# Performance work log

Measured on AMD Instinct MI355X. Metric: run time of the kernel, lower is better.

## Reference

```python
import jax, jax.numpy as jnp
import numpy as np

EPS = 1e-8  # torch.nn.CosineSimilarity default eps


def setup_inputs() -> dict:
    key = jax.random.key(0)
    k1, k2, k3 = jax.random.split(key, 3)
    B, D, C = 262144, 256, 64
    inputs = jax.random.normal(k1, (B, D), dtype=jnp.float32)
    labels = jax.random.randint(k2, (B,), 0, C, dtype=jnp.int64)
    class_avgs = jax.random.normal(k3, (C, D), dtype=jnp.float32)
    return {"inputs": inputs, "labels": labels, "class_avgs": class_avgs}


def reference(inputs, labels, class_avgs):
    # Cosine similarity of every input row against every class centroid.
    # Faithful to the original double loop: classes whose avg vector contains
    # inf get similarity 1.0 (the "unseen class" sentinel branch).
    inf_mask = jnp.any(jnp.isinf(class_avgs), axis=-1)  # (C,)
    x_norm = jnp.linalg.norm(inputs, axis=-1)           # (B,)
    c_norm = jnp.linalg.norm(class_avgs, axis=-1)       # (C,)
    dots = jnp.einsum("bd,cd->bc", inputs, class_avgs)  # (B, C)
    denom = jnp.maximum(x_norm[:, None] * c_norm[None, :], EPS)
    sims = dots / denom
    return jnp.where(inf_mask[None, :], jnp.float32(1.0), sims)
```

## Files before the change

kernel.cpp:

```cpp
#include <hip/hip_runtime.h>
#include <hip/hip_bf16.h>


typedef __attribute__((ext_vector_type(8))) short bf16x8;
typedef __attribute__((ext_vector_type(4))) float f32x4;

#define EPS 1e-8f

__device__ __forceinline__ short f2bf(float f) {
  union { float f; unsigned u; } v; v.f = f;
  unsigned r = v.u + 0x7fffu + ((v.u >> 16) & 1u);
  return (short)(r >> 16);
}

__global__ __launch_bounds__(256) void simrel_kernel(
    const float* __restrict__ X,
    const float* __restrict__ CLS,
    float* __restrict__ OUT)
{
  constexpr int D  = 256;
  constexpr int C  = 64;
  constexpr int SK = 264;

  __shared__ __align__(16) short Blds[C * SK];
  __shared__ float cn_s[C];
  __shared__ float cinf_s[C];

  const int tid = threadIdx.x;

  {
    const int c = tid >> 2;
    const int q = tid & 3;
    const float4* src = (const float4*)(CLS + c * D + q * 64);
    short* dst = &Blds[c * SK + q * 64];
    float ssq = 0.f;
    int inf = 0;
#pragma unroll
    for (int i = 0; i < 16; ++i) {
      float4 v = src[i];
      ssq += v.x * v.x + v.y * v.y;
      ssq += v.z * v.z + v.w * v.w;
      inf |= (isinf(v.x) | isinf(v.y) | isinf(v.z) | isinf(v.w));
      *(short4*)(dst + i * 4) =
          make_short4(f2bf(v.x), f2bf(v.y), f2bf(v.z), f2bf(v.w));
    }
    ssq += __shfl_xor(ssq, 1);
    ssq += __shfl_xor(ssq, 2);
    inf |= __shfl_xor(inf, 1);
    inf |= __shfl_xor(inf, 2);
    if (q == 0) {
      cn_s[c]   = sqrtf(ssq);
      cinf_s[c] = inf ? 1.f : 0.f;
    }
  }
  __syncthreads();

  const int lane = tid & 63;
  const int wave = tid >> 6;
  const int m    = lane & 15;
  const int quad = lane >> 4;

  const long rowbase = (long)blockIdx.x * 256 + wave * 64;

  const float4* Ap[4];
#pragma unroll
  for (int mt = 0; mt < 4; ++mt)
    Ap[mt] = (const float4*)X + (rowbase + mt * 16 + m) * 64 + quad * 2;

  const short* Bp[4];
#pragma unroll
  for (int nt = 0; nt < 4; ++nt)
    Bp[nt] = &Blds[(nt * 16 + m) * SK + quad * 8];

  f32x4 acc[4][4];
#pragma unroll
  for (int mt = 0; mt < 4; ++mt)
#pragma unroll
    for (int nt = 0; nt < 4; ++nt)
      acc[mt][nt] = (f32x4){0.f, 0.f, 0.f, 0.f};

  float ssqr[4] = {0.f, 0.f, 0.f, 0.f};

  float4 cur[8];
#pragma unroll
  for (int mt = 0; mt < 4; ++mt) {
    cur[2 * mt]     = Ap[mt][0];
    cur[2 * mt + 1] = Ap[mt][1];
  }

#pragma unroll
  for (int ks = 0; ks < 8; ++ks) {
    float4 nxt[8];
    if (ks < 7) {
#pragma unroll
      for (int mt = 0; mt < 4; ++mt) {
        nxt[2 * mt]     = Ap[mt][(ks + 1) * 8];
        nxt[2 * mt + 1] = Ap[mt][(ks + 1) * 8 + 1];
      }
    }

    bf16x8 bf[4];
#pragma unroll
    for (int nt = 0; nt < 4; ++nt)
      bf[nt] = *(const bf16x8*)(Bp[nt] + ks * 32);

#pragma unroll
    for (int mt = 0; mt < 4; ++mt) {
      float4 a0 = cur[2 * mt], a1 = cur[2 * mt + 1];
      ssqr[mt] += a0.x * a0.x + a0.y * a0.y + a0.z * a0.z + a0.w * a0.w +
                  a1.x * a1.x + a1.y * a1.y + a1.z * a1.z + a1.w * a1.w;
      bf16x8 af;
      af[0] = f2bf(a0.x); af[1] = f2bf(a0.y); af[2] = f2bf(a0.z); af[3] = f2bf(a0.w);
      af[4] = f2bf(a1.x); af[5] = f2bf(a1.y); af[6] = f2bf(a1.z); af[7] = f2bf(a1.w);
#pragma unroll
      for (int nt = 0; nt < 4; ++nt)
        acc[mt][nt] =
            __builtin_amdgcn_mfma_f32_16x16x32_bf16(af, bf[nt], acc[mt][nt], 0, 0, 0);
    }

    if (ks < 7) {
#pragma unroll
      for (int i = 0; i < 8; ++i) cur[i] = nxt[i];
    }
  }

#pragma unroll
  for (int mt = 0; mt < 4; ++mt) {
    float s = ssqr[mt];
    s += __shfl_xor(s, 16);
    s += __shfl_xor(s, 32);
    float xn = sqrtf(s);
    float xnr[4];
#pragma unroll
    for (int r = 0; r < 4; ++r)
      xnr[r] = __shfl(xn, quad * 4 + r);
#pragma unroll
    for (int nt = 0; nt < 4; ++nt) {
      const int n = nt * 16 + m;
      const float cn  = cn_s[n];
      const bool cinf = (cinf_s[n] != 0.f);
#pragma unroll
      for (int r = 0; r < 4; ++r) {
        const long row = rowbase + mt * 16 + quad * 4 + r;
        const float denom = fmaxf(xnr[r] * cn, EPS);
        const float v =
            cinf ? 1.0f : acc[mt][nt][r] * __builtin_amdgcn_rcpf(denom);
        OUT[row * 64 + n] = v;
      }
    }
  }
}

extern "C" void kernel_launch(void* const* d_in, const int* in_sizes, int n_in,
                              void* d_out, int out_size, void* d_ws, size_t ws_size,
                              hipStream_t stream) {
  (void)n_in; (void)d_ws; (void)ws_size; (void)out_size;
  const float* X   = (const float*)d_in[0];
  const float* CLS = (const float*)d_in[2];
  float* OUT = (float*)d_out;

  const int Brows  = in_sizes[0] / 256;
  const int blocks = Brows / 256;
  simrel_kernel<<<blocks, 256, 0, stream>>>(X, CLS, OUT);
}
```

Baseline: 392.9 us.

## Stream input rows via global_load_lds double buffer and pre-swizzle class fragments

Input tiles are now fetched straight into per-wave LDS double buffers with global_load_lds and explicit vmcnt waits, instead of register prefetch. Class centroids are stored in LDS in MFMA fragment order, and their norms and inf flags are recomputed per wave from the bf16 copies. Each block now handles 128 rows instead of 256, which lowers register pressure but repeats the centroid setup more often. Computing the centroid norm from bf16 values slightly changes accuracy.

```diff
diff --git a/kernel.cpp b/kernel.cpp
--- a/kernel.cpp
+++ b/kernel.cpp
@@ -1,5 +1,6 @@
 #include <hip/hip_runtime.h>
 #include <hip/hip_bf16.h>
+#include <math.h>
 
 
 typedef __attribute__((ext_vector_type(8))) short bf16x8;
@@ -12,121 +13,133 @@
   unsigned r = v.u + 0x7fffu + ((v.u >> 16) & 1u);
   return (short)(r >> 16);
 }
+__device__ __forceinline__ float bf2f(short s) {
+  union { float f; unsigned u; } v;
+  v.u = ((unsigned)(unsigned short)s) << 16;
+  return v.f;
+}
+
+__device__ __forceinline__ void dma16(const float* g, float* l) {
+  __builtin_amdgcn_global_load_lds(
+      (const __attribute__((address_space(1))) void*)g,
+      (__attribute__((address_space(3))) void*)l, 16, 0, 0);
+}
+
 
 __global__ __launch_bounds__(256) void simrel_kernel(
     const float* __restrict__ X,
     const float* __restrict__ CLS,
     float* __restrict__ OUT)
 {
-  constexpr int D  = 256;
-  constexpr int C  = 64;
-  constexpr int SK = 264;
+  __shared__ __align__(16) float Abuf[4 * 2048];
+  __shared__ __align__(16) short Bfrag[8 * 4 * 64 * 8];
 
-  __shared__ __align__(16) short Blds[C * SK];
-  __shared__ float cn_s[C];
-  __shared__ float cinf_s[C];
-
-  const int tid = threadIdx.x;
+  const int tid  = threadIdx.x;
+  const int wave = tid >> 6;
+  const int lane = tid & 63;
+  const int m    = lane & 15;
+  const int quad = lane >> 4;
 
   {
-    const int c = tid >> 2;
-    const int q = tid & 3;
-    const float4* src = (const float4*)(CLS + c * D + q * 64);
-    short* dst = &Blds[c * SK + q * 64];
-    float ssq = 0.f;
-    int inf = 0;
+    const int c  = tid >> 2;
+    const int qq = tid & 3;
+    const float4* src = (const float4*)CLS + c * 64 + qq * 16;
 #pragma unroll
     for (int i = 0; i < 16; ++i) {
       float4 v = src[i];
-      ssq += v.x * v.x + v.y * v.y;
-      ssq += v.z * v.z + v.w * v.w;
-      inf |= (isinf(v.x) | isinf(v.y) | isinf(v.z) | isinf(v.w));
-      *(short4*)(dst + i * 4) =
+      const int wabs = qq * 64 + i * 4;
+      const int ks = wabs >> 5;
+      const int w0 = wabs & 31;
+      const int h  = w0 >> 4;
+      const int qd = (w0 >> 2) & 3;
+      const int lb = (qd << 4) | (c & 15);
+      const int nt = c >> 4;
+      *(short4*)&Bfrag[((ks * 4 + nt) * 64 + lb) * 8 + h * 4] =
           make_short4(f2bf(v.x), f2bf(v.y), f2bf(v.z), f2bf(v.w));
-    }
-    ssq += __shfl_xor(ssq, 1);
-    ssq += __shfl_xor(ssq, 2);
-    inf |= __shfl_xor(inf, 1);
-    inf |= __shfl_xor(inf, 2);
-    if (q == 0) {
-      cn_s[c]   = sqrtf(ssq);
-      cinf_s[c] = inf ? 1.f : 0.f;
     }
   }
   __syncthreads();
 
-  const int lane = tid & 63;
-  const int wave = tid >> 6;
-  const int m    = lane & 15;
-  const int quad = lane >> 4;
+  const size_t rowbase = (size_t)blockIdx.x * 128 + (size_t)wave * 32;
 
-  const long rowbase = (long)blockIdx.x * 256 + wave * 64;
+  const float* gbase[2][2];
+#pragma unroll
+  for (int mti = 0; mti < 2; ++mti)
+#pragma unroll
+    for (int h = 0; h < 2; ++h)
+      gbase[mti][h] = X + (rowbase + mti * 16 + m) * 256 + h * 16 + quad * 4;
 
-  const float4* Ap[4];
+  float* abase = &Abuf[wave * 2048];
+
 #pragma unroll
-  for (int mt = 0; mt < 4; ++mt)
-    Ap[mt] = (const float4*)X + (rowbase + mt * 16 + m) * 64 + quad * 2;
+  for (int mti = 0; mti < 2; ++mti)
+#pragma unroll
+    for (int h = 0; h < 2; ++h)
+      dma16(gbase[mti][h], abase + (mti * 2 + h) * 256);
 
-  const short* Bp[4];
+  float cnv[4]; int cflag[4];
 #pragma unroll
-  for (int nt = 0; nt < 4; ++nt)
-    Bp[nt] = &Blds[(nt * 16 + m) * SK + quad * 8];
+  for (int nt = 0; nt < 4; ++nt) {
+    float s = 0.f;
+#pragma unroll
+    for (int ks = 0; ks < 8; ++ks) {
+      bf16x8 b = *(const bf16x8*)&Bfrag[((ks * 4 + nt) * 64 + lane) * 8];
+#pragma unroll
+      for (int j = 0; j < 8; ++j) { float f = bf2f(b[j]); s += f * f; }
+    }
+    s += __shfl_xor(s, 16);
+    s += __shfl_xor(s, 32);
+    cflag[nt] = !isfinite(s);
+    cnv[nt]   = sqrtf(s);
+  }
 
-  f32x4 acc[4][4];
+  f32x4 acc[2][4];
 #pragma unroll
-  for (int mt = 0; mt < 4; ++mt)
+  for (int mti = 0; mti < 2; ++mti)
 #pragma unroll
     for (int nt = 0; nt < 4; ++nt)
-      acc[mt][nt] = (f32x4){0.f, 0.f, 0.f, 0.f};
-
-  float ssqr[4] = {0.f, 0.f, 0.f, 0.f};
-
-  float4 cur[8];
-#pragma unroll
-  for (int mt = 0; mt < 4; ++mt) {
-    cur[2 * mt]     = Ap[mt][0];
-    cur[2 * mt + 1] = Ap[mt][1];
-  }
+      acc[mti][nt] = (f32x4){0.f, 0.f, 0.f, 0.f};
+  float ssqr[2] = {0.f, 0.f};
 
 #pragma unroll
   for (int ks = 0; ks < 8; ++ks) {
-    float4 nxt[8];
     if (ks < 7) {
+      const int nb = (ks + 1) & 1;
 #pragma unroll
-      for (int mt = 0; mt < 4; ++mt) {
-        nxt[2 * mt]     = Ap[mt][(ks + 1) * 8];
-        nxt[2 * mt + 1] = Ap[mt][(ks + 1) * 8 + 1];
-      }
+      for (int mti = 0; mti < 2; ++mti)
+#pragma unroll
+        for (int h = 0; h < 2; ++h)
+          dma16(gbase[mti][h] + (ks + 1) * 32, abase + (nb * 4 + mti * 2 + h) * 256);
+      asm volatile("s_waitcnt vmcnt(4)" ::: "memory");
+    } else {
+      asm volatile("s_waitcnt vmcnt(0)" ::: "memory");
     }
+    const int cb = ks & 1;
 
-    bf16x8 bf[4];
+    bf16x8 bw[4];
 #pragma unroll
     for (int nt = 0; nt < 4; ++nt)
-      bf[nt] = *(const bf16x8*)(Bp[nt] + ks * 32);
+      bw[nt] = *(const bf16x8*)&Bfrag[((ks * 4 + nt) * 64 + lane) * 8];
 
 #pragma unroll
-    for (int mt = 0; mt < 4; ++mt) {
-      float4 a0 = cur[2 * mt], a1 = cur[2 * mt + 1];
-      ssqr[mt] += a0.x * a0.x + a0.y * a0.y + a0.z * a0.z + a0.w * a0.w +
-                  a1.x * a1.x + a1.y * a1.y + a1.z * a1.z + a1.w * a1.w;
+    for (int mti = 0; mti < 2; ++mti) {
+      float4 a0 = *(const float4*)(abase + (cb * 4 + mti * 2 + 0) * 256 + lane * 4);
+      float4 a1 = *(const float4*)(abase + (cb * 4 + mti * 2 + 1) * 256 + lane * 4);
+      ssqr[mti] += a0.x * a0.x + a0.y * a0.y + a0.z * a0.z + a0.w * a0.w +
+                   a1.x * a1.x + a1.y * a1.y + a1.z * a1.z + a1.w * a1.w;
       bf16x8 af;
       af[0] = f2bf(a0.x); af[1] = f2bf(a0.y); af[2] = f2bf(a0.z); af[3] = f2bf(a0.w);
       af[4] = f2bf(a1.x); af[5] = f2bf(a1.y); af[6] = f2bf(a1.z); af[7] = f2bf(a1.w);
 #pragma unroll
       for (int nt = 0; nt < 4; ++nt)
-        acc[mt][nt] =
-            __builtin_amdgcn_mfma_f32_16x16x32_bf16(af, bf[nt], acc[mt][nt], 0, 0, 0);
-    }
-
-    if (ks < 7) {
-#pragma unroll
-      for (int i = 0; i < 8; ++i) cur[i] = nxt[i];
+        acc[mti][nt] =
+            __builtin_amdgcn_mfma_f32_16x16x32_bf16(af, bw[nt], acc[mti][nt], 0, 0, 0);
     }
   }
 
 #pragma unroll
-  for (int mt = 0; mt < 4; ++mt) {
-    float s = ssqr[mt];
+  for (int mti = 0; mti < 2; ++mti) {
+    float s = ssqr[mti];
     s += __shfl_xor(s, 16);
     s += __shfl_xor(s, 32);
     float xn = sqrtf(s);
@@ -137,14 +150,12 @@
 #pragma unroll
     for (int nt = 0; nt < 4; ++nt) {
       const int n = nt * 16 + m;
-      const float cn  = cn_s[n];
-      const bool cinf = (cinf_s[n] != 0.f);
 #pragma unroll
       for (int r = 0; r < 4; ++r) {
-        const long row = rowbase + mt * 16 + quad * 4 + r;
-        const float denom = fmaxf(xnr[r] * cn, EPS);
+        const size_t row = rowbase + mti * 16 + quad * 4 + r;
+        const float d = fmaxf(xnr[r] * cnv[nt], EPS);
         const float v =
-            cinf ? 1.0f : acc[mt][nt][r] * __builtin_amdgcn_rcpf(denom);
+            cflag[nt] ? 1.0f : acc[mti][nt][r] * __builtin_amdgcn_rcpf(d);
         OUT[row * 64 + n] = v;
       }
     }
@@ -160,6 +171,6 @@
   float* OUT = (float*)d_out;
 
   const int Brows  = in_sizes[0] / 256;
-  const int blocks = Brows / 256;
+  const int blocks = Brows / 128;
   simrel_kernel<<<blocks, 256, 0, stream>>>(X, CLS, OUT);
 }
```

New measurement: 385.5 us. Within noise of the previous version (-1.9%).
